# Performance work log

Hardware: AMD Instinct MI355X
Metric: run time of the kernel (lower is better)

## Reference

```python
import jax, jax.numpy as jnp
import numpy as np

B, L, H, E = 32, 512, 8, 64  # L == S == win_size, D == E

def setup_inputs() -> dict:
    key = jax.random.key(0)
    kq, kk, kv, ks = jax.random.split(key, 4)
    return {
        "queries": jax.random.normal(kq, (B, L, H, E), dtype=jnp.float32),
        "keys":    jax.random.normal(kk, (B, L, H, E), dtype=jnp.float32),
        "values":  jax.random.normal(kv, (B, L, H, E), dtype=jnp.float32),
        "sigma":   jax.random.normal(ks, (B, L, H), dtype=jnp.float32),
    }

def reference(queries, keys, values, sigma):
    b, l, h, e = queries.shape
    scale = 1.0 / np.sqrt(e).astype(np.float32)
    # scores: [B,H,L,S]
    attn = scale * jnp.einsum('blhe,bshe->bhls', queries, keys)
    # learned sigma -> Gaussian prior
    sig = jnp.transpose(sigma, (0, 2, 1))            # [B,H,L]
    sig = jax.nn.sigmoid(sig * 5.0) + 1e-5
    sig = jnp.power(3.0, sig) - 1.0
    sig = sig[..., None]                             # [B,H,L,1], broadcast over S (no repeat)
    idx = jnp.arange(l, dtype=jnp.float32)
    dist = jnp.abs(idx[:, None] - idx[None, :])      # [L,S] |i-j| distances buffer
    inv_sqrt_2pi = 1.0 / np.sqrt(2.0 * np.pi).astype(np.float32)
    prior = (inv_sqrt_2pi / sig) * jnp.exp(-(dist ** 2) / (2.0 * sig ** 2))  # [B,H,L,S]
    series = jax.nn.softmax(attn, axis=-1)           # dropout p=0.0 -> identity
    V = jnp.einsum('bhls,bshd->blhd', series, values)
    return V, series, prior
```

## Files before the change

kernel.cpp:

```cpp
#include <hip/hip_runtime.h>
#include <math.h>

#define Bc 32
#define Lc 512
#define Hc 8
#define Ec 64
#define Sc 512

typedef __attribute__((ext_vector_type(8))) _Float16 f16x8;
typedef __attribute__((ext_vector_type(4))) _Float16 f16x4;
typedef __attribute__((ext_vector_type(4))) float    f32x4;

__global__ __launch_bounds__(256) void pack_k(const float* __restrict__ src,
                                              _Float16* __restrict__ dst) {
    const int t = threadIdx.x;
    const int b = blockIdx.z, h = blockIdx.y, s0 = blockIdx.x * 32;
    const int e4 = (t & 15) * 4;
    const int sr = t >> 4;
    #pragma unroll
    for (int i = 0; i < 2; ++i) {
        const int s = s0 + sr + 16 * i;
        const float4 v = *(const float4*)&src[(((size_t)b * Lc + s) * Hc + h) * Ec + e4];
        f16x4 o;
        o[0] = (_Float16)v.x; o[1] = (_Float16)v.y;
        o[2] = (_Float16)v.z; o[3] = (_Float16)v.w;
        *(f16x4*)&dst[(((size_t)b * Hc + h) * Lc + s) * Ec + e4] = o;
    }
}

__global__ __launch_bounds__(256) void pack_vt(const float* __restrict__ V,
                                               _Float16* __restrict__ Vt) {
    __shared__ float LT[64 * 68];
    const int t = threadIdx.x;
    const int b = blockIdx.z, h = blockIdx.y, s0 = blockIdx.x * 64;
    #pragma unroll
    for (int i = 0; i < 16; ++i) {
        const int idx = t + 256 * i;
        const int e = idx & 63, s = idx >> 6;
        LT[e * 68 + s] = V[(((size_t)b * Lc + s0 + s) * Hc + h) * Ec + e];
    }
    __syncthreads();
    #pragma unroll
    for (int i = 0; i < 16; ++i) {
        const int idx = t + 256 * i;
        const int s = idx & 63, e = idx >> 6;
        Vt[((size_t)(b * Hc + h) * Ec + e) * Sc + s0 + s] = (_Float16)LT[e * 68 + s];
    }
}

__global__ __launch_bounds__(256) void prior_kernel(
    const float* __restrict__ sigma, float* __restrict__ prior)
{
    const int wave = threadIdx.x >> 6;
    const int lane = threadIdx.x & 63;
    const int row  = blockIdx.x * 4 + wave;
    const int l    = row & (Lc - 1);
    const int bh   = row >> 9;
    const int b    = bh >> 3;
    const int h    = bh & (Hc - 1);

    float sg = sigma[((size_t)b * Lc + l) * Hc + h];
    sg = 1.0f / (1.0f + __expf(-5.0f * sg)) + 1e-5f;
    sg = expm1f(sg * 1.0986122886681098f);
    const float inv = 0.3989422804014327f / sg;
    const float c2  = -0.5f / (sg * sg);

    const size_t base = (size_t)row * Sc;
    #pragma unroll
    for (int i = 0; i < 2; ++i) {
        const int s0 = i * 256 + lane * 4;
        const float d0 = (float)(l - (s0 + 0));
        const float d1 = (float)(l - (s0 + 1));
        const float d2 = (float)(l - (s0 + 2));
        const float d3 = (float)(l - (s0 + 3));
        f32x4 o;
        o[0] = inv * __expf(c2 * d0 * d0);
        o[1] = inv * __expf(c2 * d1 * d1);
        o[2] = inv * __expf(c2 * d2 * d2);
        o[3] = inv * __expf(c2 * d3 * d3);
        __builtin_nontemporal_store(o, (f32x4*)&prior[base + s0]);
    }
}

__global__ __launch_bounds__(256, 4) void attn_mfma(
    const float* __restrict__ Q, const _Float16* __restrict__ Kh,
    const _Float16* __restrict__ Vt,
    float* __restrict__ outV, float* __restrict__ series)
{
    __shared__ float smx[4][16];
    __shared__ float ssm[4][16];
    __shared__ float ex[2][64][16];

    const int t    = threadIdx.x;
    const int lane = t & 63, wave = t >> 6;
    const int quad = lane >> 4, l16 = lane & 15;
    const int hs   = wave & 1;
    const int rg   = wave >> 1;

    const int bid = blockIdx.x;
    const int xcd = bid & 7;
    const int rr  = bid >> 3;
    const int xt  = rr & 15;
    const int bh  = (rr >> 4) * 8 + xcd;
    const int b = bh >> 3, h = bh & 7;
    const int l0 = xt * 32;
    const int l  = l0 + rg * 16 + l16;

    const size_t kb = (size_t)bh * Lc * Ec;
    const int sbase = hs * 256;

    f16x8 qf[2];
    {
        const float* qp = &Q[(((size_t)b * Lc + l) * Hc + h) * Ec + quad * 8];
        #pragma unroll
        for (int kt = 0; kt < 2; ++kt) {
            const float4 v0 = *(const float4*)(qp + kt * 32);
            const float4 v1 = *(const float4*)(qp + kt * 32 + 4);
            qf[kt][0] = (_Float16)v0.x; qf[kt][1] = (_Float16)v0.y;
            qf[kt][2] = (_Float16)v0.z; qf[kt][3] = (_Float16)v0.w;
            qf[kt][4] = (_Float16)v1.x; qf[kt][5] = (_Float16)v1.y;
            qf[kt][6] = (_Float16)v1.z; qf[kt][7] = (_Float16)v1.w;
        }
    }

    f32x4 acc[16];
    #pragma unroll
    for (int nt = 0; nt < 16; ++nt) { acc[nt][0]=0.f; acc[nt][1]=0.f; acc[nt][2]=0.f; acc[nt][3]=0.f; }

    const int arow = (l16 >> 2) * 8 + (l16 & 3);
    #pragma unroll
    for (int nt = 0; nt < 16; ++nt) {
        const int s = sbase + (nt >> 1) * 32 + arow + (nt & 1) * 4;
        const _Float16* kp = &Kh[kb + (size_t)s * Ec + quad * 8];
        #pragma unroll
        for (int kt = 0; kt < 2; ++kt) {
            const f16x8 kf = *(const f16x8*)(kp + kt * 32);
            acc[nt] = __builtin_amdgcn_mfma_f32_16x16x32_f16(kf, qf[kt], acc[nt], 0, 0, 0);
        }
    }

    float mx = acc[0][0];
    #pragma unroll
    for (int nt = 0; nt < 16; ++nt) {
        #pragma unroll
        for (int r4 = 0; r4 < 4; ++r4) mx = fmaxf(mx, acc[nt][r4]);
    }
    mx = fmaxf(mx, __shfl_xor(mx, 16));
    mx = fmaxf(mx, __shfl_xor(mx, 32));
    if (lane < 16) smx[wave][lane] = mx;
    __syncthreads();
    mx = fmaxf(mx, smx[wave ^ 1][l16]);

    float ssum = 0.f;
    #pragma unroll
    for (int nt = 0; nt < 16; ++nt) {
        #pragma unroll
        for (int r4 = 0; r4 < 4; ++r4) {
            const float e = __expf((acc[nt][r4] - mx) * 0.125f);
            acc[nt][r4] = e; ssum += e;
        }
    }
    ssum += __shfl_xor(ssum, 16);
    ssum += __shfl_xor(ssum, 32);
    if (lane < 16) ssm[wave][lane] = ssum;
    __syncthreads();
    ssum += ssm[wave ^ 1][l16];
    const float is = 1.f / ssum;
    #pragma unroll
    for (int nt = 0; nt < 16; ++nt) {
        acc[nt][0] *= is; acc[nt][1] *= is; acc[nt][2] *= is; acc[nt][3] *= is;
    }

    f32x4 oaccT[4];
    #pragma unroll
    for (int et = 0; et < 4; ++et) { oaccT[et][0]=0.f; oaccT[et][1]=0.f; oaccT[et][2]=0.f; oaccT[et][3]=0.f; }

    const _Float16* vb = &Vt[(size_t)bh * Ec * Sc];
    float* srow = &series[((size_t)bh * Lc + l) * Sc + sbase];
    #pragma unroll
    for (int t2 = 0; t2 < 8; ++t2) {
        const f32x4 p0 = acc[2 * t2];
        const f32x4 p1 = acc[2 * t2 + 1];
        __builtin_nontemporal_store(p0, (f32x4*)&srow[t2 * 32 + quad * 8]);
        __builtin_nontemporal_store(p1, (f32x4*)&srow[t2 * 32 + quad * 8 + 4]);
        f16x8 pb;
        pb[0] = (_Float16)p0[0]; pb[1] = (_Float16)p0[1];
        pb[2] = (_Float16)p0[2]; pb[3] = (_Float16)p0[3];
        pb[4] = (_Float16)p1[0]; pb[5] = (_Float16)p1[1];
        pb[6] = (_Float16)p1[2]; pb[7] = (_Float16)p1[3];
        #pragma unroll
        for (int et = 0; et < 4; ++et) {
            const f16x8 vf = *(const f16x8*)&vb[(size_t)(et * 16 + l16) * Sc + sbase + t2 * 32 + quad * 8];
            oaccT[et] = __builtin_amdgcn_mfma_f32_16x16x32_f16(vf, pb, oaccT[et], 0, 0, 0);
        }
    }

    if (hs == 1) {
        #pragma unroll
        for (int et = 0; et < 4; ++et)
            *(f32x4*)&ex[rg][lane][et * 4] = oaccT[et];
    }
    __syncthreads();
    if (hs == 0) {
        #pragma unroll
        for (int et = 0; et < 4; ++et) {
            const f32x4 p = *(const f32x4*)&ex[rg][lane][et * 4];
            f32x4 o;
            o[0] = oaccT[et][0] + p[0]; o[1] = oaccT[et][1] + p[1];
            o[2] = oaccT[et][2] + p[2]; o[3] = oaccT[et][3] + p[3];
            __builtin_nontemporal_store(o,
                (f32x4*)&outV[(((size_t)b * Lc + l) * Hc + h) * Ec + et * 16 + quad * 4]);
        }
    }
}

extern "C" void kernel_launch(void* const* d_in, const int* in_sizes, int n_in,
                              void* d_out, int out_size, void* d_ws, size_t ws_size,
                              hipStream_t stream) {
    (void)n_in; (void)in_sizes; (void)out_size; (void)d_ws; (void)ws_size;
    const float* Q  = (const float*)d_in[0];
    const float* K  = (const float*)d_in[1];
    const float* Vv = (const float*)d_in[2];
    const float* sg = (const float*)d_in[3];

    float* outV   = (float*)d_out;
    float* series = outV + (size_t)Bc * Lc * Hc * Ec;
    float* prior  = series + (size_t)Bc * Hc * Lc * Sc;

    const size_t plane = (size_t)Bc * Hc * Lc * Ec;
    _Float16* Kh = (_Float16*)prior;
    _Float16* Vt = Kh + plane;

    pack_k <<<dim3(Lc / 32, Hc, Bc), 256, 0, stream>>>(K, Kh);
    pack_vt<<<dim3(Lc / 64, Hc, Bc), 256, 0, stream>>>(Vv, Vt);
    attn_mfma<<<dim3((Bc * Hc * Lc) / 32, 1, 1), 256, 0, stream>>>(
        Q, Kh, Vt, outV, series);
    prior_kernel<<<(Bc * Hc * Lc) / 4, 256, 0, stream>>>(sg, prior);
}
```

Baseline: 747.5 us.

## Fuse prior generation into attention kernel, merge pack kernels, single-sync softmax

The K and V packing kernels are merged into one launch that branches on block index. The separate prior kernel is mostly folded into the tail of the attention kernel. Each attention block writes prior rows for its bh, except the first 32 bh, whose prior region is reused as the fp16 K/V scratch; a small tail kernel writes those afterwards. The softmax now exchanges max and sum together across the two half-row waves and rescales the sums, removing one block barrier. The aim is to cut launch overhead and overlap prior stores with attention work, at the cost of more per-block work and register pressure in the attention kernel.

```diff
diff --git a/kernel.cpp b/kernel.cpp
--- a/kernel.cpp
+++ b/kernel.cpp
@@ -11,44 +11,63 @@
 typedef __attribute__((ext_vector_type(4))) _Float16 f16x4;
 typedef __attribute__((ext_vector_type(4))) float    f32x4;
 
-__global__ __launch_bounds__(256) void pack_k(const float* __restrict__ src,
-                                              _Float16* __restrict__ dst) {
-    const int t = threadIdx.x;
-    const int b = blockIdx.z, h = blockIdx.y, s0 = blockIdx.x * 32;
-    const int e4 = (t & 15) * 4;
-    const int sr = t >> 4;
-    #pragma unroll
-    for (int i = 0; i < 2; ++i) {
-        const int s = s0 + sr + 16 * i;
-        const float4 v = *(const float4*)&src[(((size_t)b * Lc + s) * Hc + h) * Ec + e4];
-        f16x4 o;
-        o[0] = (_Float16)v.x; o[1] = (_Float16)v.y;
-        o[2] = (_Float16)v.z; o[3] = (_Float16)v.w;
-        *(f16x4*)&dst[(((size_t)b * Hc + h) * Lc + s) * Ec + e4] = o;
-    }
-}
-
-__global__ __launch_bounds__(256) void pack_vt(const float* __restrict__ V,
+__device__ inline void prior_row(float sg_raw, int lrow, int lane, float* pp) {
+    float sg = 1.0f / (1.0f + __expf(-5.0f * sg_raw)) + 1e-5f;
+    sg = expm1f(sg * 1.0986122886681098f);
+    const float inv = 0.3989422804014327f / sg;
+    const float c2  = -0.5f / (sg * sg);
+    const int c0 = lane * 8;
+    f32x4 o0, o1;
+    #pragma unroll
+    for (int j = 0; j < 4; ++j) {
+        const float d0 = (float)(lrow - (c0 + j));
+        const float d1 = (float)(lrow - (c0 + 4 + j));
+        o0[j] = inv * __expf(c2 * d0 * d0);
+        o1[j] = inv * __expf(c2 * d1 * d1);
+    }
+    __builtin_nontemporal_store(o0, (f32x4*)(pp + c0));
+    __builtin_nontemporal_store(o1, (f32x4*)(pp + c0 + 4));
+}
+
+__global__ __launch_bounds__(256) void pack_kv(const float* __restrict__ K,
+                                               const float* __restrict__ V,
+                                               _Float16* __restrict__ Kh,
                                                _Float16* __restrict__ Vt) {
     __shared__ float LT[64 * 68];
     const int t = threadIdx.x;
-    const int b = blockIdx.z, h = blockIdx.y, s0 = blockIdx.x * 64;
-    #pragma unroll
-    for (int i = 0; i < 16; ++i) {
-        const int idx = t + 256 * i;
-        const int e = idx & 63, s = idx >> 6;
-        LT[e * 68 + s] = V[(((size_t)b * Lc + s0 + s) * Hc + h) * Ec + e];
-    }
-    __syncthreads();
-    #pragma unroll
-    for (int i = 0; i < 16; ++i) {
-        const int idx = t + 256 * i;
-        const int s = idx & 63, e = idx >> 6;
-        Vt[((size_t)(b * Hc + h) * Ec + e) * Sc + s0 + s] = (_Float16)LT[e * 68 + s];
-    }
-}
-
-__global__ __launch_bounds__(256) void prior_kernel(
+    const int b = blockIdx.z, h = blockIdx.y;
+    if (blockIdx.x < 16) {
+        const int s0 = blockIdx.x * 32;
+        const int e4 = (t & 15) * 4;
+        const int sr = t >> 4;
+        #pragma unroll
+        for (int i = 0; i < 2; ++i) {
+            const int s = s0 + sr + 16 * i;
+            const float4 v = *(const float4*)&K[(((size_t)b * Lc + s) * Hc + h) * Ec + e4];
+            f16x4 o;
+            o[0] = (_Float16)v.x; o[1] = (_Float16)v.y;
+            o[2] = (_Float16)v.z; o[3] = (_Float16)v.w;
+            *(f16x4*)&Kh[(((size_t)b * Hc + h) * Lc + s) * Ec + e4] = o;
+        }
+    } else {
+        const int s0 = (blockIdx.x - 16) * 64;
+        #pragma unroll
+        for (int i = 0; i < 16; ++i) {
+            const int idx = t + 256 * i;
+            const int e = idx & 63, s = idx >> 6;
+            LT[e * 68 + s] = V[(((size_t)b * Lc + s0 + s) * Hc + h) * Ec + e];
+        }
+        __syncthreads();
+        #pragma unroll
+        for (int i = 0; i < 16; ++i) {
+            const int idx = t + 256 * i;
+            const int s = idx & 63, e = idx >> 6;
+            Vt[((size_t)(b * Hc + h) * Ec + e) * Sc + s0 + s] = (_Float16)LT[e * 68 + s];
+        }
+    }
+}
+
+__global__ __launch_bounds__(256) void prior_tail(
     const float* __restrict__ sigma, float* __restrict__ prior)
 {
     const int wave = threadIdx.x >> 6;
@@ -58,38 +77,16 @@
     const int bh   = row >> 9;
     const int b    = bh >> 3;
     const int h    = bh & (Hc - 1);
-
-    float sg = sigma[((size_t)b * Lc + l) * Hc + h];
-    sg = 1.0f / (1.0f + __expf(-5.0f * sg)) + 1e-5f;
-    sg = expm1f(sg * 1.0986122886681098f);
-    const float inv = 0.3989422804014327f / sg;
-    const float c2  = -0.5f / (sg * sg);
-
-    const size_t base = (size_t)row * Sc;
-    #pragma unroll
-    for (int i = 0; i < 2; ++i) {
-        const int s0 = i * 256 + lane * 4;
-        const float d0 = (float)(l - (s0 + 0));
-        const float d1 = (float)(l - (s0 + 1));
-        const float d2 = (float)(l - (s0 + 2));
-        const float d3 = (float)(l - (s0 + 3));
-        f32x4 o;
-        o[0] = inv * __expf(c2 * d0 * d0);
-        o[1] = inv * __expf(c2 * d1 * d1);
-        o[2] = inv * __expf(c2 * d2 * d2);
-        o[3] = inv * __expf(c2 * d3 * d3);
-        __builtin_nontemporal_store(o, (f32x4*)&prior[base + s0]);
-    }
+    prior_row(sigma[((size_t)b * Lc + l) * Hc + h], l, lane, &prior[(size_t)row * Sc]);
 }
 
 __global__ __launch_bounds__(256, 4) void attn_mfma(
     const float* __restrict__ Q, const _Float16* __restrict__ Kh,
-    const _Float16* __restrict__ Vt,
-    float* __restrict__ outV, float* __restrict__ series)
+    const _Float16* __restrict__ Vt, const float* __restrict__ sigma,
+    float* __restrict__ outV, float* __restrict__ series, float* __restrict__ prior)
 {
-    __shared__ float smx[4][16];
-    __shared__ float ssm[4][16];
-    __shared__ float ex[2][64][16];
+    __shared__ float2 pairs[4][16];
+    __shared__ float  ex[2][64][16];
 
     const int t    = threadIdx.x;
     const int lane = t & 63, wave = t >> 6;
@@ -147,9 +144,6 @@
     }
     mx = fmaxf(mx, __shfl_xor(mx, 16));
     mx = fmaxf(mx, __shfl_xor(mx, 32));
-    if (lane < 16) smx[wave][lane] = mx;
-    __syncthreads();
-    mx = fmaxf(mx, smx[wave ^ 1][l16]);
 
     float ssum = 0.f;
     #pragma unroll
@@ -162,10 +156,13 @@
     }
     ssum += __shfl_xor(ssum, 16);
     ssum += __shfl_xor(ssum, 32);
-    if (lane < 16) ssm[wave][lane] = ssum;
+    if (lane < 16) pairs[wave][lane] = make_float2(mx, ssum);
     __syncthreads();
-    ssum += ssm[wave ^ 1][l16];
-    const float is = 1.f / ssum;
+    const float2 o2 = pairs[wave ^ 1][l16];
+    const float m   = fmaxf(mx, o2.x);
+    const float w0  = __expf((mx   - m) * 0.125f);
+    const float w1  = __expf((o2.x - m) * 0.125f);
+    const float is  = w0 / (ssum * w0 + o2.y * w1);
     #pragma unroll
     for (int nt = 0; nt < 16; ++nt) {
         acc[nt][0] *= is; acc[nt][1] *= is; acc[nt][2] *= is; acc[nt][3] *= is;
@@ -212,6 +209,15 @@
                 (f32x4*)&outV[(((size_t)b * Lc + l) * Hc + h) * Ec + et * 16 + quad * 4]);
         }
     }
+
+    if (bh >= 32) {
+        #pragma unroll
+        for (int r_ = 0; r_ < 8; ++r_) {
+            const int lrow = l0 + wave * 8 + r_;
+            prior_row(sigma[((size_t)b * Lc + lrow) * Hc + h], lrow, lane,
+                      &prior[((size_t)bh * Lc + lrow) * Sc]);
+        }
+    }
 }
 
 extern "C" void kernel_launch(void* const* d_in, const int* in_sizes, int n_in,
@@ -231,9 +237,8 @@
     _Float16* Kh = (_Float16*)prior;
     _Float16* Vt = Kh + plane;
 
-    pack_k <<<dim3(Lc / 32, Hc, Bc), 256, 0, stream>>>(K, Kh);
-    pack_vt<<<dim3(Lc / 64, Hc, Bc), 256, 0, stream>>>(Vv, Vt);
+    pack_kv<<<dim3(24, Hc, Bc), 256, 0, stream>>>(K, Vv, Kh, Vt);
     attn_mfma<<<dim3((Bc * Hc * Lc) / 32, 1, 1), 256, 0, stream>>>(
-        Q, Kh, Vt, outV, series);
-    prior_kernel<<<(Bc * Hc * Lc) / 4, 256, 0, stream>>>(sg, prior);
-}
+        Q, Kh, Vt, sg, outV, series, prior);
+    prior_tail<<<(32 * Lc) / 4, 256, 0, stream>>>(sg, prior);
+}
```

Measured after the change: 782.2 us. 1.05x slower.

## Give each wave a full score row and merge the K and V pack kernels

Applied to the files above, without the earlier changes.

Each wave now covers all 512 key columns for its 16 query rows, with 64 rows per block, instead of two waves splitting the key range. This removes the shared-memory max, sum and output exchanges and their barriers. The cost is a 32-tile accumulator per wave and launch bounds lowered to two blocks per CU, so occupancy drops. The two packing kernels are also merged into one launch to save a kernel launch.

```diff
diff --git a/kernel.cpp b/kernel.cpp
--- a/kernel.cpp
+++ b/kernel.cpp
@@ -11,40 +11,41 @@
 typedef __attribute__((ext_vector_type(4))) _Float16 f16x4;
 typedef __attribute__((ext_vector_type(4))) float    f32x4;
 
-__global__ __launch_bounds__(256) void pack_k(const float* __restrict__ src,
-                                              _Float16* __restrict__ dst) {
-    const int t = threadIdx.x;
-    const int b = blockIdx.z, h = blockIdx.y, s0 = blockIdx.x * 32;
-    const int e4 = (t & 15) * 4;
-    const int sr = t >> 4;
-    #pragma unroll
-    for (int i = 0; i < 2; ++i) {
-        const int s = s0 + sr + 16 * i;
-        const float4 v = *(const float4*)&src[(((size_t)b * Lc + s) * Hc + h) * Ec + e4];
-        f16x4 o;
-        o[0] = (_Float16)v.x; o[1] = (_Float16)v.y;
-        o[2] = (_Float16)v.z; o[3] = (_Float16)v.w;
-        *(f16x4*)&dst[(((size_t)b * Hc + h) * Lc + s) * Ec + e4] = o;
-    }
-}
-
-__global__ __launch_bounds__(256) void pack_vt(const float* __restrict__ V,
+__global__ __launch_bounds__(256) void pack_kv(const float* __restrict__ K,
+                                               const float* __restrict__ V,
+                                               _Float16* __restrict__ Kh,
                                                _Float16* __restrict__ Vt) {
     __shared__ float LT[64 * 68];
     const int t = threadIdx.x;
-    const int b = blockIdx.z, h = blockIdx.y, s0 = blockIdx.x * 64;
-    #pragma unroll
-    for (int i = 0; i < 16; ++i) {
-        const int idx = t + 256 * i;
-        const int e = idx & 63, s = idx >> 6;
-        LT[e * 68 + s] = V[(((size_t)b * Lc + s0 + s) * Hc + h) * Ec + e];
-    }
-    __syncthreads();
-    #pragma unroll
-    for (int i = 0; i < 16; ++i) {
-        const int idx = t + 256 * i;
-        const int s = idx & 63, e = idx >> 6;
-        Vt[((size_t)(b * Hc + h) * Ec + e) * Sc + s0 + s] = (_Float16)LT[e * 68 + s];
+    const int b = blockIdx.z, h = blockIdx.y;
+    if (blockIdx.x < 16) {
+        const int s0 = blockIdx.x * 32;
+        const int e4 = (t & 15) * 4;
+        const int sr = t >> 4;
+        #pragma unroll
+        for (int i = 0; i < 2; ++i) {
+            const int s = s0 + sr + 16 * i;
+            const float4 v = *(const float4*)&K[(((size_t)b * Lc + s) * Hc + h) * Ec + e4];
+            f16x4 o;
+            o[0] = (_Float16)v.x; o[1] = (_Float16)v.y;
+            o[2] = (_Float16)v.z; o[3] = (_Float16)v.w;
+            *(f16x4*)&Kh[(((size_t)b * Hc + h) * Lc + s) * Ec + e4] = o;
+        }
+    } else {
+        const int s0 = (blockIdx.x - 16) * 64;
+        #pragma unroll
+        for (int i = 0; i < 16; ++i) {
+            const int idx = t + 256 * i;
+            const int e = idx & 63, s = idx >> 6;
+            LT[e * 68 + s] = V[(((size_t)b * Lc + s0 + s) * Hc + h) * Ec + e];
+        }
+        __syncthreads();
+        #pragma unroll
+        for (int i = 0; i < 16; ++i) {
+            const int idx = t + 256 * i;
+            const int s = idx & 63, e = idx >> 6;
+            Vt[((size_t)(b * Hc + h) * Ec + e) * Sc + s0 + s] = (_Float16)LT[e * 68 + s];
+        }
     }
 }
 
@@ -82,32 +83,24 @@
     }
 }
 
-__global__ __launch_bounds__(256, 4) void attn_mfma(
+__global__ __launch_bounds__(256, 2) void attn_mfma(
     const float* __restrict__ Q, const _Float16* __restrict__ Kh,
     const _Float16* __restrict__ Vt,
     float* __restrict__ outV, float* __restrict__ series)
 {
-    __shared__ float smx[4][16];
-    __shared__ float ssm[4][16];
-    __shared__ float ex[2][64][16];
-
     const int t    = threadIdx.x;
     const int lane = t & 63, wave = t >> 6;
     const int quad = lane >> 4, l16 = lane & 15;
-    const int hs   = wave & 1;
-    const int rg   = wave >> 1;
 
     const int bid = blockIdx.x;
     const int xcd = bid & 7;
     const int rr  = bid >> 3;
-    const int xt  = rr & 15;
-    const int bh  = (rr >> 4) * 8 + xcd;
+    const int xt  = rr & 7;
+    const int bh  = (rr >> 3) * 8 + xcd;
     const int b = bh >> 3, h = bh & 7;
-    const int l0 = xt * 32;
-    const int l  = l0 + rg * 16 + l16;
+    const int l  = xt * 64 + wave * 16 + l16;
 
     const size_t kb = (size_t)bh * Lc * Ec;
-    const int sbase = hs * 256;
 
     f16x8 qf[2];
     {
@@ -123,14 +116,14 @@
         }
     }
 
-    f32x4 acc[16];
-    #pragma unroll
-    for (int nt = 0; nt < 16; ++nt) { acc[nt][0]=0.f; acc[nt][1]=0.f; acc[nt][2]=0.f; acc[nt][3]=0.f; }
+    f32x4 acc[32];
+    #pragma unroll
+    for (int nt = 0; nt < 32; ++nt) { acc[nt][0]=0.f; acc[nt][1]=0.f; acc[nt][2]=0.f; acc[nt][3]=0.f; }
 
     const int arow = (l16 >> 2) * 8 + (l16 & 3);
     #pragma unroll
-    for (int nt = 0; nt < 16; ++nt) {
-        const int s = sbase + (nt >> 1) * 32 + arow + (nt & 1) * 4;
+    for (int nt = 0; nt < 32; ++nt) {
+        const int s = (nt >> 1) * 32 + arow + (nt & 1) * 4;
         const _Float16* kp = &Kh[kb + (size_t)s * Ec + quad * 8];
         #pragma unroll
         for (int kt = 0; kt < 2; ++kt) {
@@ -141,19 +134,15 @@
 
     float mx = acc[0][0];
     #pragma unroll
-    for (int nt = 0; nt < 16; ++nt) {
+    for (int nt = 0; nt < 32; ++nt) {
         #pragma unroll
         for (int r4 = 0; r4 < 4; ++r4) mx = fmaxf(mx, acc[nt][r4]);
     }
     mx = fmaxf(mx, __shfl_xor(mx, 16));
     mx = fmaxf(mx, __shfl_xor(mx, 32));
-    if (lane < 16) smx[wave][lane] = mx;
-    __syncthreads();
-    mx = fmaxf(mx, smx[wave ^ 1][l16]);
-
     float ssum = 0.f;
     #pragma unroll
-    for (int nt = 0; nt < 16; ++nt) {
+    for (int nt = 0; nt < 32; ++nt) {
         #pragma unroll
         for (int r4 = 0; r4 < 4; ++r4) {
             const float e = __expf((acc[nt][r4] - mx) * 0.125f);
@@ -162,12 +151,9 @@
     }
     ssum += __shfl_xor(ssum, 16);
     ssum += __shfl_xor(ssum, 32);
-    if (lane < 16) ssm[wave][lane] = ssum;
-    __syncthreads();
-    ssum += ssm[wave ^ 1][l16];
     const float is = 1.f / ssum;
     #pragma unroll
-    for (int nt = 0; nt < 16; ++nt) {
+    for (int nt = 0; nt < 32; ++nt) {
         acc[nt][0] *= is; acc[nt][1] *= is; acc[nt][2] *= is; acc[nt][3] *= is;
     }
 
@@ -176,9 +162,9 @@
     for (int et = 0; et < 4; ++et) { oaccT[et][0]=0.f; oaccT[et][1]=0.f; oaccT[et][2]=0.f; oaccT[et][3]=0.f; }
 
     const _Float16* vb = &Vt[(size_t)bh * Ec * Sc];
-    float* srow = &series[((size_t)bh * Lc + l) * Sc + sbase];
-    #pragma unroll
-    for (int t2 = 0; t2 < 8; ++t2) {
+    float* srow = &series[((size_t)bh * Lc + l) * Sc];
+    #pragma unroll
+    for (int t2 = 0; t2 < 16; ++t2) {
         const f32x4 p0 = acc[2 * t2];
         const f32x4 p1 = acc[2 * t2 + 1];
         __builtin_nontemporal_store(p0, (f32x4*)&srow[t2 * 32 + quad * 8]);
@@ -190,27 +176,15 @@
         pb[6] = (_Float16)p1[2]; pb[7] = (_Float16)p1[3];
         #pragma unroll
         for (int et = 0; et < 4; ++et) {
-            const f16x8 vf = *(const f16x8*)&vb[(size_t)(et * 16 + l16) * Sc + sbase + t2 * 32 + quad * 8];
+            const f16x8 vf = *(const f16x8*)&vb[(size_t)(et * 16 + l16) * Sc + t2 * 32 + quad * 8];
             oaccT[et] = __builtin_amdgcn_mfma_f32_16x16x32_f16(vf, pb, oaccT[et], 0, 0, 0);
         }
     }
 
-    if (hs == 1) {
-        #pragma unroll
-        for (int et = 0; et < 4; ++et)
-            *(f32x4*)&ex[rg][lane][et * 4] = oaccT[et];
-    }
-    __syncthreads();
-    if (hs == 0) {
-        #pragma unroll
-        for (int et = 0; et < 4; ++et) {
-            const f32x4 p = *(const f32x4*)&ex[rg][lane][et * 4];
-            f32x4 o;
-            o[0] = oaccT[et][0] + p[0]; o[1] = oaccT[et][1] + p[1];
-            o[2] = oaccT[et][2] + p[2]; o[3] = oaccT[et][3] + p[3];
-            __builtin_nontemporal_store(o,
-                (f32x4*)&outV[(((size_t)b * Lc + l) * Hc + h) * Ec + et * 16 + quad * 4]);
-        }
+    #pragma unroll
+    for (int et = 0; et < 4; ++et) {
+        __builtin_nontemporal_store(oaccT[et],
+            (f32x4*)&outV[(((size_t)b * Lc + l) * Hc + h) * Ec + et * 16 + quad * 4]);
     }
 }
 
@@ -231,9 +205,8 @@
     _Float16* Kh = (_Float16*)prior;
     _Float16* Vt = Kh + plane;
 
-    pack_k <<<dim3(Lc / 32, Hc, Bc), 256, 0, stream>>>(K, Kh);
-    pack_vt<<<dim3(Lc / 64, Hc, Bc), 256, 0, stream>>>(Vv, Vt);
-    attn_mfma<<<dim3((Bc * Hc * Lc) / 32, 1, 1), 256, 0, stream>>>(
+    pack_kv<<<dim3(24, Hc, Bc), 256, 0, stream>>>(K, Vv, Kh, Vt);
+    attn_mfma<<<dim3((Bc * Hc * Lc) / 64, 1, 1), 256, 0, stream>>>(
         Q, Kh, Vt, outV, series);
     prior_kernel<<<(Bc * Hc * Lc) / 4, 256, 0, stream>>>(sg, prior);
 }
```

After: 713.7 us. -4.5%, faster.
